# Kernel tuning notes

Measured on AMD Instinct MI355X. Metric: run time of the kernel, lower is better.

The kernel has to match this reference:

```python
import jax, jax.numpy as jnp
import numpy as np

N_EMBD = 1024  # C; source scales scores by C**-0.5 (n_embd, not head_size)


def setup_inputs() -> dict:
    key = jax.random.key(0)
    kx, kk, kq, kv = jax.random.split(key, 4)
    B, T, C, H = 8, 2048, N_EMBD, 64
    x = jax.random.normal(kx, (B, T, C), dtype=jnp.float32)
    Wk = jax.random.normal(kk, (C, H), dtype=jnp.float32) * (C ** -0.5)
    Wq = jax.random.normal(kq, (C, H), dtype=jnp.float32) * (C ** -0.5)
    Wv = jax.random.normal(kv, (C, H), dtype=jnp.float32) * (C ** -0.5)
    return {"x": x, "Wk": Wk, "Wq": Wq, "Wv": Wv}


def reference(x, Wk, Wq, Wv):
    B, T, C = x.shape
    k = jnp.einsum('btc,ch->bth', x, Wk)
    q = jnp.einsum('btc,ch->bth', x, Wq)
    v = jnp.einsum('btc,ch->bth', x, Wv)
    # scores scaled by C**-0.5 (faithful to source, which uses n_embd not head_size)
    wei = jnp.einsum('bth,bsh->bts', q, k) * (C ** -0.5)  # [B,T,T]
    causal = jnp.tril(jnp.ones((T, T), dtype=bool))
    wei = jnp.where(causal, wei, -jnp.inf)
    wei = jax.nn.softmax(wei, axis=-1)
    # dropout is identity in eval mode
    out = jnp.einsum('bts,bsh->bth', wei, v)
    return out
```

## Files before the change

kernel.cpp:

```cpp
#include <hip/hip_runtime.h>


#define B_ 8
#define T_ 2048
#define C_ 1024
#define H_ 64
#define BTH (B_ * T_ * H_)

typedef unsigned short u16;
typedef float f32x4 __attribute__((ext_vector_type(4)));
typedef __bf16 bf16x8 __attribute__((ext_vector_type(8)));
#define AS1 __attribute__((address_space(1)))
#define AS3 __attribute__((address_space(3)))

__device__ __forceinline__ u16 f2bf(float f) {
  union { float f; unsigned u; } c; c.f = f;
  unsigned u = c.u;
  return (u16)((u + 0x7FFFu + ((u >> 16) & 1u)) >> 16);
}

__device__ __forceinline__ bf16x8 cvt8(const float4 a, const float4 b) {
  bf16x8 r;
  r[0] = (__bf16)a.x; r[1] = (__bf16)a.y; r[2] = (__bf16)a.z; r[3] = (__bf16)a.w;
  r[4] = (__bf16)b.x; r[5] = (__bf16)b.y; r[6] = (__bf16)b.z; r[7] = (__bf16)b.w;
  return r;
}

__global__ __launch_bounds__(256)
void wpack(const float* __restrict__ Wk, const float* __restrict__ Wq,
           const float* __restrict__ Wv, u16* __restrict__ Wct) {
  const int g  = blockIdx.x;
  const int k0 = blockIdx.y * 64;
  const float* __restrict__ W = (g == 0) ? Wk : (g == 1) ? Wq : Wv;
#pragma unroll
  for (int it = 0; it < 16; ++it) {
    const int idx = it * 256 + threadIdx.x;
    const int kk = k0 + (idx >> 6), h = idx & 63;
    Wct[(size_t)(g * 64 + h) * C_ + kk] = f2bf(W[(size_t)kk * H_ + h]);
  }
}

__global__ __launch_bounds__(256, 5)
void qkv_gemm(const float* __restrict__ x, const u16* __restrict__ Wct,
              u16* __restrict__ ws) {
  __shared__ u16 Bs[192 * 64];
  __shared__ u16 Xs[32 * 64];
  const int tid  = threadIdx.x;
  const int wv   = tid >> 6, lane = tid & 63;
  const int l15 = lane & 15, quad = lane >> 4;
  const int r0 = blockIdx.x * 32;
  const int xrow = tid >> 3, xcp = tid & 7;
  const float* __restrict__ xsrc = x + (size_t)(r0 + xrow) * C_ + xcp * 8;
  u16* const xdst = &Xs[xrow * 64 + ((xcp ^ (xrow & 7)) * 8)];
  const int cksw = l15 & 7;
  const f32x4 z = {0.f, 0.f, 0.f, 0.f};
  f32x4 acc[2][3];
#pragma unroll
  for (int m = 0; m < 2; ++m)
#pragma unroll
    for (int ni = 0; ni < 3; ++ni) acc[m][ni] = z;

  float4 xr0 = *(const float4*)(xsrc);
  float4 xr1 = *(const float4*)(xsrc + 4);
#pragma unroll
  for (int it = 0; it < 6; ++it) {
    const int slot = it * 256 + tid;
    const int row = slot >> 3, cp = slot & 7;
    __builtin_amdgcn_global_load_lds(
        (const AS1 unsigned*)(Wct + (size_t)row * C_ + ((cp ^ (row & 7)) * 8)),
        (AS3 unsigned*)(&Bs[slot * 8]), 16, 0, 0);
  }
  *(bf16x8*)xdst = cvt8(xr0, xr1);
  __syncthreads();

#pragma unroll 1
  for (int st = 0; st < 16; ++st) {
    if (st < 15) {
      xr0 = *(const float4*)(xsrc + (st + 1) * 64);
      xr1 = *(const float4*)(xsrc + (st + 1) * 64 + 4);
    }
#pragma unroll
    for (int kk = 0; kk < 2; ++kk) {
      const int co = ((kk * 4 + quad) ^ cksw) * 8;
      const bf16x8 a0 = *(const bf16x8*)(&Xs[l15 * 64 + co]);
      const bf16x8 a1 = *(const bf16x8*)(&Xs[(16 + l15) * 64 + co]);
#pragma unroll
      for (int ni = 0; ni < 3; ++ni) {
        const bf16x8 b = *(const bf16x8*)(&Bs[(wv * 48 + ni * 16 + l15) * 64 + co]);
        acc[0][ni] = __builtin_amdgcn_mfma_f32_16x16x32_bf16(a0, b, acc[0][ni], 0, 0, 0);
        acc[1][ni] = __builtin_amdgcn_mfma_f32_16x16x32_bf16(a1, b, acc[1][ni], 0, 0, 0);
      }
    }
    __syncthreads();
    if (st < 15) {
      const int k1 = (st + 1) * 64;
#pragma unroll
      for (int it = 0; it < 6; ++it) {
        const int slot = it * 256 + tid;
        const int row = slot >> 3, cp = slot & 7;
        __builtin_amdgcn_global_load_lds(
            (const AS1 unsigned*)(Wct + (size_t)row * C_ + k1 + ((cp ^ (row & 7)) * 8)),
            (AS3 unsigned*)(&Bs[slot * 8]), 16, 0, 0);
      }
      *(bf16x8*)xdst = cvt8(xr0, xr1);
    }
    __syncthreads();
  }

  const float SCLL = 0.03125f * 1.44269504088896f;
#pragma unroll
  for (int m = 0; m < 2; ++m) {
    const int rowg = r0 + m * 16;
    const int bb = rowg >> 11;
    const int tb = (rowg & 2047) + quad * 4;
#pragma unroll
    for (int ni = 0; ni < 3; ++ni) {
      const int col = wv * 48 + ni * 16 + l15;
      const int g = col >> 6, h = col & 63;
      f32x4 a = acc[m][ni];
      if (g == 1) { a[0] *= SCLL; a[1] *= SCLL; a[2] *= SCLL; a[3] *= SCLL; }
      if (g < 2) {
        u16* op = ws + (size_t)g * BTH + (size_t)(rowg + quad * 4) * H_ + h;
#pragma unroll
        for (int r = 0; r < 4; ++r) op[(size_t)r * H_] = f2bf(a[r]);
      } else {
        uint2 pk;
        pk.x = (unsigned)f2bf(a[0]) | ((unsigned)f2bf(a[1]) << 16);
        pk.y = (unsigned)f2bf(a[2]) | ((unsigned)f2bf(a[3]) << 16);
        *(uint2*)(ws + (size_t)2 * BTH + (size_t)(bb * H_ + h) * T_ + tb) = pk;
      }
    }
  }
}

__global__ __launch_bounds__(256)
void flash(const u16* __restrict__ ws, float* __restrict__ fpart) {
  __shared__ u16 Ks[2][64 * 64];
  __shared__ u16 Vs[2][64 * 64];
  __shared__ __bf16 Pt[4][16 * 72];
  const u16* __restrict__ kg = ws;
  const u16* __restrict__ qg = ws + BTH;
  const u16* __restrict__ vt = ws + (size_t)2 * BTH;
  const int b  = blockIdx.y;
  const int bx = 143 - (int)blockIdx.x;
  int c = 0;
#pragma unroll
  for (int t = 1; t < 8; ++t)
    if (34 * t - 2 * t * t <= bx) c = t;
  const int u = 4 * c + (bx - (34 * c - 2 * c * c));
  const int tid  = threadIdx.x;
  const int wv   = tid >> 6;
  const int lane = tid & 63;
  const int l15  = lane & 15, quad = lane >> 4;
  const int qt   = 4 * u + wv;
  const int t0   = qt * 16;
  const int st0  = 4 * c;
  const int stE  = (st0 + 4 < u + 1) ? st0 + 4 : u + 1;
  const u16* kb0 = kg + (size_t)b * T_ * H_;
  const u16* vb0 = vt + (size_t)b * H_ * T_;
  const int srow = tid >> 3, scp = tid & 7;
  const u16* qrow = qg + ((size_t)(b * T_ + t0 + l15)) * H_ + quad * 8;
  const bf16x8 qf0 = *(const bf16x8*)qrow;
  const bf16x8 qf1 = *(const bf16x8*)(qrow + 32);
  __bf16* pt = &Pt[wv][0];
  const f32x4 z = {0.f, 0.f, 0.f, 0.f};
  f32x4 o[4];
  float lr[4] = {0.f, 0.f, 0.f, 0.f};
#pragma unroll
  for (int hi = 0; hi < 4; ++hi) o[hi] = z;

  {
    const int s00 = st0 * 64;
#pragma unroll
    for (int jj = 0; jj < 2; ++jj) {
      const int row = jj * 32 + srow;
      const int sc  = scp ^ (row & 7);
      __builtin_amdgcn_global_load_lds(
          (const AS1 unsigned*)(kb0 + (size_t)(s00 + row) * H_ + sc * 8),
          (AS3 unsigned*)(&Ks[0][(jj * 256 + tid) * 8]), 16, 0, 0);
      __builtin_amdgcn_global_load_lds(
          (const AS1 unsigned*)(vb0 + (size_t)row * T_ + s00 + sc * 8),
          (AS3 unsigned*)(&Vs[0][(jj * 256 + tid) * 8]), 16, 0, 0);
    }
  }
  __syncthreads();

#pragma unroll 1
  for (int st = st0; st < stE; ++st) {
    const int cur = (st - st0) & 1;
    if (st + 1 < stE) {
      const int s1 = (st + 1) * 64;
#pragma unroll
      for (int jj = 0; jj < 2; ++jj) {
        const int row = jj * 32 + srow;
        const int sc  = scp ^ (row & 7);
        __builtin_amdgcn_global_load_lds(
            (const AS1 unsigned*)(kb0 + (size_t)(s1 + row) * H_ + sc * 8),
            (AS3 unsigned*)(&Ks[cur ^ 1][(jj * 256 + tid) * 8]), 16, 0, 0);
        __builtin_amdgcn_global_load_lds(
            (const AS1 unsigned*)(vb0 + (size_t)row * T_ + s1 + sc * 8),
            (AS3 unsigned*)(&Vs[cur ^ 1][(jj * 256 + tid) * 8]), 16, 0, 0);
      }
    }
    const u16* Kc = &Ks[cur][0];
    const u16* Vc = &Vs[cur][0];
    const int sw = (l15 & 7);
    f32x4 s[4];
#pragma unroll
    for (int ni = 0; ni < 4; ++ni) {
      const u16* kr = Kc + (ni * 16 + l15) * 64;
      const bf16x8 k0 = *(const bf16x8*)(kr + ((quad       ^ sw) * 8));
      const bf16x8 k1 = *(const bf16x8*)(kr + (((4 + quad) ^ sw) * 8));
      s[ni] = __builtin_amdgcn_mfma_f32_16x16x32_bf16(qf0, k0, z, 0, 0, 0);
      s[ni] = __builtin_amdgcn_mfma_f32_16x16x32_bf16(qf1, k1, s[ni], 0, 0, 0);
    }
    if (st == u) {
      const int s0 = st * 64;
#pragma unroll
      for (int ni = 0; ni < 4; ++ni)
#pragma unroll
        for (int r = 0; r < 4; ++r)
          if (s0 + ni * 16 + l15 > t0 + quad * 4 + r) s[ni][r] = -1e30f;
    }
    float p[4][4];
#pragma unroll
    for (int ni = 0; ni < 4; ++ni)
#pragma unroll
      for (int r = 0; r < 4; ++r) p[ni][r] = __builtin_amdgcn_exp2f(s[ni][r]);
#pragma unroll
    for (int r = 0; r < 4; ++r)
      lr[r] += (p[0][r] + p[1][r]) + (p[2][r] + p[3][r]);
#pragma unroll
    for (int ni = 0; ni < 4; ++ni)
#pragma unroll
      for (int r = 0; r < 4; ++r)
        pt[(quad * 4 + r) * 72 + ni * 16 + l15] = (__bf16)p[ni][r];
    asm volatile("s_waitcnt lgkmcnt(0)" ::: "memory");
    const bf16x8 pa0 = *(const bf16x8*)(pt + l15 * 72 + quad * 8);
    const bf16x8 pa1 = *(const bf16x8*)(pt + l15 * 72 + 32 + quad * 8);
    asm volatile("" ::: "memory");
#pragma unroll
    for (int hi = 0; hi < 4; ++hi) {
      const u16* vr = Vc + (hi * 16 + l15) * 64;
      const bf16x8 v0 = *(const bf16x8*)(vr + ((quad       ^ sw) * 8));
      const bf16x8 v1 = *(const bf16x8*)(vr + (((4 + quad) ^ sw) * 8));
      o[hi] = __builtin_amdgcn_mfma_f32_16x16x32_bf16(pa0, v0, o[hi], 0, 0, 0);
      o[hi] = __builtin_amdgcn_mfma_f32_16x16x32_bf16(pa1, v1, o[hi], 0, 0, 0);
    }
    __syncthreads();
  }
#pragma unroll
  for (int d = 1; d < 16; d <<= 1)
#pragma unroll
    for (int r = 0; r < 4; ++r) lr[r] += __shfl_xor(lr[r], d, 64);
  float* po = fpart + (size_t)((b * 128 + qt) * 8 + c) * 1040;
#pragma unroll
  for (int hi = 0; hi < 4; ++hi)
#pragma unroll
    for (int r = 0; r < 4; ++r)
      po[(quad * 4 + r) * 64 + hi * 16 + l15] = o[hi][r];
  if (l15 == 0) {
#pragma unroll
    for (int r = 0; r < 4; ++r) po[1024 + quad * 4 + r] = lr[r];
  }
}

__global__ __launch_bounds__(256)
void freduce(const float* __restrict__ fpart, float* __restrict__ out) {
  const int qt  = blockIdx.x;
  const int b   = blockIdx.y;
  const int tid = threadIdx.x;
  const int nc  = (qt >> 4) + 1;
  const float* __restrict__ pb = fpart + (size_t)(b * 128 + qt) * 8 * 1040;
  __shared__ float ls[16];
  if (tid < 16) {
    float s = 0.f;
#pragma unroll 1
    for (int i = 0; i < nc; ++i) s += pb[(size_t)i * 1040 + 1024 + tid];
    ls[tid] = s;
  }
  __syncthreads();
  f32x4 a = {0.f, 0.f, 0.f, 0.f};
#pragma unroll 1
  for (int i = 0; i < nc; ++i)
    a += *(const f32x4*)(pb + (size_t)i * 1040 + tid * 4);
  const float inv = 1.0f / ls[tid >> 4];
  a[0] *= inv; a[1] *= inv; a[2] *= inv; a[3] *= inv;
  *(f32x4*)(out + (size_t)(b * T_ + qt * 16 + (tid >> 4)) * H_ + ((tid * 4) & 63)) = a;
}

extern "C" void kernel_launch(void* const* d_in, const int* in_sizes, int n_in,
                              void* d_out, int out_size, void* d_ws, size_t ws_size,
                              hipStream_t stream) {
  const float* x  = (const float*)d_in[0];
  const float* Wk = (const float*)d_in[1];
  const float* Wq = (const float*)d_in[2];
  const float* Wv = (const float*)d_in[3];
  u16*   ws  = (u16*)d_ws;
  u16*   Wct = ws + (size_t)3 * BTH;
  float* fpart = (float*)(ws + (size_t)3 * BTH + 192 * 1024);
  float* out = (float*)d_out;
  wpack<<<dim3(3, 16), 256, 0, stream>>>(Wk, Wq, Wv, Wct);
  qkv_gemm<<<dim3(512), 256, 0, stream>>>(x, Wct, ws);
  flash<<<dim3(144, B_), 256, 0, stream>>>(ws, fpart);
  freduce<<<dim3(128, B_), 256, 0, stream>>>(fpart, out);
}
```

Baseline: 137.3 us.

## Double-buffer LDS tiles in QKV GEMM with explicit vmcnt waits

Converts the QKV projection GEMM from a single-buffered LDS loop with two barriers per K-step to a double-buffered pipeline. The next W tile (via global_load_lds) and the next x slice are issued before computing on the current buffer, with explicit s_waitcnt vmcnt and one barrier per step. The last step is peeled off. This doubles LDS use and lowers the launch-bounds occupancy hint from 5 to 2, so fewer blocks may be resident to hide latency. The hand-counted vmcnt values must exactly match the number of outstanding loads.

```diff
diff --git a/kernel.cpp b/kernel.cpp
--- a/kernel.cpp
+++ b/kernel.cpp
@@ -25,6 +25,17 @@
   r[4] = (__bf16)b.x; r[5] = (__bf16)b.y; r[6] = (__bf16)b.z; r[7] = (__bf16)b.w;
   return r;
 }
+
+#define WAIT_VM(N) do {                                         \
+    asm volatile("s_waitcnt vmcnt(" #N ")" ::: "memory");       \
+    __builtin_amdgcn_sched_barrier(0);                          \
+  } while (0)
+
+#define LBAR() do {                                             \
+    asm volatile("s_waitcnt lgkmcnt(0)" ::: "memory");          \
+    __builtin_amdgcn_s_barrier();                               \
+    __builtin_amdgcn_sched_barrier(0);                          \
+  } while (0)
 
 __global__ __launch_bounds__(256)
 void wpack(const float* __restrict__ Wk, const float* __restrict__ Wq,
@@ -40,18 +51,18 @@
   }
 }
 
-__global__ __launch_bounds__(256, 5)
+__global__ __launch_bounds__(256, 2)
 void qkv_gemm(const float* __restrict__ x, const u16* __restrict__ Wct,
               u16* __restrict__ ws) {
-  __shared__ u16 Bs[192 * 64];
-  __shared__ u16 Xs[32 * 64];
+  __shared__ u16 Bs[2][192 * 64];
+  __shared__ u16 Xs[2][32 * 64];
   const int tid  = threadIdx.x;
   const int wv   = tid >> 6, lane = tid & 63;
   const int l15 = lane & 15, quad = lane >> 4;
   const int r0 = blockIdx.x * 32;
   const int xrow = tid >> 3, xcp = tid & 7;
   const float* __restrict__ xsrc = x + (size_t)(r0 + xrow) * C_ + xcp * 8;
-  u16* const xdst = &Xs[xrow * 64 + ((xcp ^ (xrow & 7)) * 8)];
+  const int xwo = xrow * 64 + ((xcp ^ (xrow & 7)) * 8);
   const int cksw = l15 & 7;
   const f32x4 z = {0.f, 0.f, 0.f, 0.f};
   f32x4 acc[2][3];
@@ -68,43 +79,56 @@
     const int row = slot >> 3, cp = slot & 7;
     __builtin_amdgcn_global_load_lds(
         (const AS1 unsigned*)(Wct + (size_t)row * C_ + ((cp ^ (row & 7)) * 8)),
-        (AS3 unsigned*)(&Bs[slot * 8]), 16, 0, 0);
-  }
-  *(bf16x8*)xdst = cvt8(xr0, xr1);
-  __syncthreads();
+        (AS3 unsigned*)(&Bs[0][slot * 8]), 16, 0, 0);
+  }
+  WAIT_VM(6);
+  *(bf16x8*)(&Xs[0][xwo]) = cvt8(xr0, xr1);
+  LBAR();
 
 #pragma unroll 1
-  for (int st = 0; st < 16; ++st) {
-    if (st < 15) {
-      xr0 = *(const float4*)(xsrc + (st + 1) * 64);
-      xr1 = *(const float4*)(xsrc + (st + 1) * 64 + 4);
-    }
+  for (int st = 0; st < 15; ++st) {
+    const int cur = st & 1;
+    const int k1 = (st + 1) * 64;
+    xr0 = *(const float4*)(xsrc + k1);
+    xr1 = *(const float4*)(xsrc + k1 + 4);
+#pragma unroll
+    for (int it = 0; it < 6; ++it) {
+      const int slot = it * 256 + tid;
+      const int row = slot >> 3, cp = slot & 7;
+      __builtin_amdgcn_global_load_lds(
+          (const AS1 unsigned*)(Wct + (size_t)row * C_ + k1 + ((cp ^ (row & 7)) * 8)),
+          (AS3 unsigned*)(&Bs[cur ^ 1][slot * 8]), 16, 0, 0);
+    }
+    WAIT_VM(8);
 #pragma unroll
     for (int kk = 0; kk < 2; ++kk) {
       const int co = ((kk * 4 + quad) ^ cksw) * 8;
-      const bf16x8 a0 = *(const bf16x8*)(&Xs[l15 * 64 + co]);
-      const bf16x8 a1 = *(const bf16x8*)(&Xs[(16 + l15) * 64 + co]);
+      const bf16x8 a0 = *(const bf16x8*)(&Xs[cur][l15 * 64 + co]);
+      const bf16x8 a1 = *(const bf16x8*)(&Xs[cur][(16 + l15) * 64 + co]);
 #pragma unroll
       for (int ni = 0; ni < 3; ++ni) {
-        const bf16x8 b = *(const bf16x8*)(&Bs[(wv * 48 + ni * 16 + l15) * 64 + co]);
+        const bf16x8 b = *(const bf16x8*)(&Bs[cur][(wv * 48 + ni * 16 + l15) * 64 + co]);
         acc[0][ni] = __builtin_amdgcn_mfma_f32_16x16x32_bf16(a0, b, acc[0][ni], 0, 0, 0);
         acc[1][ni] = __builtin_amdgcn_mfma_f32_16x16x32_bf16(a1, b, acc[1][ni], 0, 0, 0);
       }
     }
-    __syncthreads();
-    if (st < 15) {
-      const int k1 = (st + 1) * 64;
-#pragma unroll
-      for (int it = 0; it < 6; ++it) {
-        const int slot = it * 256 + tid;
-        const int row = slot >> 3, cp = slot & 7;
-        __builtin_amdgcn_global_load_lds(
-            (const AS1 unsigned*)(Wct + (size_t)row * C_ + k1 + ((cp ^ (row & 7)) * 8)),
-            (AS3 unsigned*)(&Bs[slot * 8]), 16, 0, 0);
-      }
-      *(bf16x8*)xdst = cvt8(xr0, xr1);
-    }
-    __syncthreads();
+    WAIT_VM(6);
+    *(bf16x8*)(&Xs[cur ^ 1][xwo]) = cvt8(xr0, xr1);
+    LBAR();
+  }
+  WAIT_VM(0);
+  __builtin_amdgcn_s_barrier();
+#pragma unroll
+  for (int kk = 0; kk < 2; ++kk) {
+    const int co = ((kk * 4 + quad) ^ cksw) * 8;
+    const bf16x8 a0 = *(const bf16x8*)(&Xs[1][l15 * 64 + co]);
+    const bf16x8 a1 = *(const bf16x8*)(&Xs[1][(16 + l15) * 64 + co]);
+#pragma unroll
+    for (int ni = 0; ni < 3; ++ni) {
+      const bf16x8 b = *(const bf16x8*)(&Bs[1][(wv * 48 + ni * 16 + l15) * 64 + co]);
+      acc[0][ni] = __builtin_amdgcn_mfma_f32_16x16x32_bf16(a0, b, acc[0][ni], 0, 0, 0);
+      acc[1][ni] = __builtin_amdgcn_mfma_f32_16x16x32_bf16(a1, b, acc[1][ni], 0, 0, 0);
+    }
   }
 
   const float SCLL = 0.03125f * 1.44269504088896f;
```

Result: slower. 147.5 us (+7.4%).
